# Kernel tuning notes

Measured on AMD Instinct MI355X. Metric: run time of the kernel, lower is better.

## Reference

```python
import jax, jax.numpy as jnp
import numpy as np

NUM_TILES = 32
N_HEAD = 4
D_MODEL = 256


def build_key_indices(n):
    # Mirrors the torch __init__ loop: row+column neighbors of token i on an n x n grid.
    key_indices = []
    for i in range(n * n):
        idx = []
        start = i // n
        end = i % n
        for j in range(n):
            idx.append(start * n + j)
            idx.append(end + n * j)
        idx.remove(i)  # i appears twice; one occurrence remains, matching torch
        key_indices.append(sorted(idx))
    return np.asarray(key_indices, dtype=np.int32)  # [T, 2n-1]


def setup_inputs() -> dict:
    key = jax.random.key(0)
    ks = jax.random.split(key, 5)
    B, T, D = 4, NUM_TILES ** 2, D_MODEL
    K = 2 * NUM_TILES - 1
    x = jax.random.normal(ks[0], (B, T, D), jnp.float32)
    scale = 1.0 / np.sqrt(D)
    Wq = jax.random.normal(ks[1], (D, D), jnp.float32) * scale  # [out, in] torch layout
    Wk = jax.random.normal(ks[2], (D, D), jnp.float32) * scale
    Wv = jax.random.normal(ks[3], (D, D), jnp.float32) * scale
    lim = np.sqrt(6.0 / (T + K))  # xavier_uniform
    wbias = jax.random.uniform(ks[4], (T, K), jnp.float32, -lim, lim)
    key_indices = jnp.asarray(build_key_indices(NUM_TILES))
    return {"x": x, "Wq": Wq, "Wk": Wk, "Wv": Wv, "wbias": wbias,
            "key_indices": key_indices}


def reference(x, Wq, Wk, Wv, wbias, key_indices):
    B, T, D = x.shape
    H = N_HEAD
    d = D // H
    # projections (torch Linear: x @ W.T), split heads -> [B,H,T,d]
    q = (x @ Wq.T).reshape(B, T, H, d).transpose(0, 2, 1, 3)
    k = (x @ Wk.T).reshape(B, T, H, d).transpose(0, 2, 1, 3)
    v = (x @ Wv.T).reshape(B, T, H, d).transpose(0, 2, 1, 3)

    ew = jnp.exp(wbias)          # [T, K]
    ek = jnp.exp(k)              # [B,H,T,d]
    kv = ek * v                  # [B,H,T,d]

    kv_g = kv[:, :, key_indices, :]   # gather -> [B,H,T,K,d]
    ek_g = ek[:, :, key_indices, :]   # gather -> [B,H,T,K,d]

    num = jnp.einsum('tk,bhtkd->bhtd', ew, kv_g)
    den = jnp.einsum('tk,bhtkd->bhtd', ew, ek_g)
    weighted = num / den

    out = jax.nn.sigmoid(q) * weighted          # [B,H,T,d]
    return out.transpose(0, 2, 1, 3).reshape(B, T, D)
```

## Files before the change

kernel.cpp:

```cpp
#include <hip/hip_runtime.h>
#include <math.h>

#define TT   1024
#define DD   256
#define KN   63
#define BB   4
#define MM   (BB * TT)

__global__ __launch_bounds__(256) void proj_kernel(
    const float* __restrict__ x,
    const float* __restrict__ Wq,
    const float* __restrict__ Wk,
    const float* __restrict__ Wv,
    float* __restrict__ P,
    float* __restrict__ EK,
    float* __restrict__ V)
{
    const int z = blockIdx.z;
    const float* __restrict__ W = (z == 0) ? Wq : (z == 1) ? Wk : Wv;
    float* __restrict__ outbuf  = (z == 0) ? P  : (z == 1) ? EK : V;

    __shared__ float xs[64][65];
    __shared__ float ws[64][65];

    const int tid = threadIdx.x;
    const int tx  = tid & 15;
    const int ty  = tid >> 4;
    const int m0  = blockIdx.x * 64;
    const int n0  = blockIdx.y * 64;

    float acc[4][4] = {};

    for (int kk = 0; kk < DD; kk += 64) {
        #pragma unroll
        for (int i = 0; i < 4; ++i) {
            const int l  = tid + 256 * i;
            const int r  = l >> 4;
            const int c4 = l & 15;
            float4 a = *reinterpret_cast<const float4*>(
                &x[(size_t)(m0 + r) * DD + kk + c4 * 4]);
            xs[r][c4 * 4 + 0] = a.x; xs[r][c4 * 4 + 1] = a.y;
            xs[r][c4 * 4 + 2] = a.z; xs[r][c4 * 4 + 3] = a.w;
            float4 b = *reinterpret_cast<const float4*>(
                &W[(size_t)(n0 + r) * DD + kk + c4 * 4]);
            ws[r][c4 * 4 + 0] = b.x; ws[r][c4 * 4 + 1] = b.y;
            ws[r][c4 * 4 + 2] = b.z; ws[r][c4 * 4 + 3] = b.w;
        }
        __syncthreads();

        #pragma unroll
        for (int k = 0; k < 64; ++k) {
            float a[4], b[4];
            #pragma unroll
            for (int i = 0; i < 4; ++i) a[i] = xs[ty * 4 + i][k];
            #pragma unroll
            for (int j = 0; j < 4; ++j) b[j] = ws[tx * 4 + j][k];
            #pragma unroll
            for (int i = 0; i < 4; ++i)
                #pragma unroll
                for (int j = 0; j < 4; ++j)
                    acc[i][j] += a[i] * b[j];
        }
        __syncthreads();
    }

    #pragma unroll
    for (int i = 0; i < 4; ++i) {
        const int r = m0 + ty * 4 + i;
        #pragma unroll
        for (int j = 0; j < 4; ++j) {
            const int c = n0 + tx * 4 + j;
            float v = acc[i][j];
            if (z == 0)      v = 1.0f / (1.0f + __expf(-v));
            else if (z == 1) v = __expf(v);
            outbuf[(size_t)r * DD + c] = v;
        }
    }
}

__global__ __launch_bounds__(256) void gather_kernel(
    const float* __restrict__ P,
    const float* __restrict__ EK,
    const float* __restrict__ V,
    const float* __restrict__ wbias,
    const int*   __restrict__ kidx,
    float* __restrict__ out)
{
    const int bt  = blockIdx.x;
    const int b   = bt >> 10;
    const int t   = bt & (TT - 1);
    const int tid = threadIdx.x;

    __shared__ float ews[KN];
    __shared__ int   idxs[KN];
    if (tid < KN) {
        ews[tid]  = __expf(wbias[t * KN + tid]);
        idxs[tid] = kidx[t * KN + tid];
    }
    __syncthreads();

    const size_t bbase = (size_t)b * TT * DD;
    float num = 0.0f, den = 0.0f;

    #pragma unroll 7
    for (int k = 0; k < KN; ++k) {
        const float  w    = ews[k];
        const size_t base = bbase + (size_t)idxs[k] * DD + tid;
        const float  e    = EK[base];
        const float  v    = V[base];
        den += w * e;
        num += w * e * v;
    }

    const size_t o = bbase + (size_t)t * DD + tid;
    out[o] = P[o] * num / den;
}

extern "C" void kernel_launch(void* const* d_in, const int* in_sizes, int n_in,
                              void* d_out, int out_size, void* d_ws, size_t ws_size,
                              hipStream_t stream) {
    const float* x     = (const float*)d_in[0];
    const float* Wq    = (const float*)d_in[1];
    const float* Wk    = (const float*)d_in[2];
    const float* Wv    = (const float*)d_in[3];
    const float* wbias = (const float*)d_in[4];
    const int*   kidx  = (const int*)d_in[5];
    float* out = (float*)d_out;

    float* P  = (float*)d_ws;
    float* EK = P  + (size_t)MM * DD;
    float* V  = EK + (size_t)MM * DD;

    dim3 g1(MM / 64, DD / 64, 3);
    proj_kernel<<<g1, dim3(256), 0, stream>>>(x, Wq, Wk, Wv, P, EK, V);

    gather_kernel<<<dim3(MM), dim3(256), 0, stream>>>(P, EK, V, wbias, kidx, out);
}
```

Baseline: 127.1 us.

## Use split-bf16 MFMA projections and separable row/column neighbor aggregation

Replaces the FP32 SIMT projection GEMM with bf16 MFMA, splitting inputs into high and low parts and using three products to keep near-FP32 accuracy. The per-token gather over 63 neighbours becomes a row pass and a column pass that stage a grid row or column in LDS and reuse it across 32 tokens. A prep kernel scatters exp(wbias) into dense row and column weight matrices. This adds two kernel launches and extra conversion traffic, and relies on the key indices having the row-plus-column grid structure, which the prep kernel decodes from kidx.

```diff
diff --git a/kernel.cpp b/kernel.cpp
--- a/kernel.cpp
+++ b/kernel.cpp
@@ -1,4 +1,5 @@
 #include <hip/hip_runtime.h>
+#include <hip/hip_bf16.h>
 #include <math.h>
 
 #define TT   1024
@@ -6,114 +7,268 @@
 #define KN   63
 #define BB   4
 #define MM   (BB * TT)
-
-__global__ __launch_bounds__(256) void proj_kernel(
-    const float* __restrict__ x,
-    const float* __restrict__ Wq,
-    const float* __restrict__ Wk,
-    const float* __restrict__ Wv,
-    float* __restrict__ P,
-    float* __restrict__ EK,
-    float* __restrict__ V)
-{
-    const int z = blockIdx.z;
-    const float* __restrict__ W = (z == 0) ? Wq : (z == 1) ? Wk : Wv;
-    float* __restrict__ outbuf  = (z == 0) ? P  : (z == 1) ? EK : V;
-
-    __shared__ float xs[64][65];
-    __shared__ float ws[64][65];
-
+#define NW   768
+
+typedef short bf16x8 __attribute__((ext_vector_type(8)));
+typedef float f32x4  __attribute__((ext_vector_type(4)));
+
+__device__ __forceinline__ unsigned short bf16bits(float f) {
+    __hip_bfloat16 h = __float2bfloat16(f);
+    return *reinterpret_cast<unsigned short*>(&h);
+}
+__device__ __forceinline__ float bf16tof(unsigned short u) {
+    __hip_bfloat16 h;
+    *reinterpret_cast<unsigned short*>(&h) = u;
+    return __bfloat162float(h);
+}
+
+__global__ __launch_bounds__(256) void prep_kernel(
+    const float* __restrict__ x,  const float* __restrict__ Wq,
+    const float* __restrict__ Wk, const float* __restrict__ Wv,
+    const float* __restrict__ wbias, const int* __restrict__ kidx,
+    __hip_bfloat16* __restrict__ xh, __hip_bfloat16* __restrict__ xl,
+    __hip_bfloat16* __restrict__ Wh, __hip_bfloat16* __restrict__ Wl,
+    float* __restrict__ Aw, float* __restrict__ Bw)
+{
+    const int bid = blockIdx.x, tid = threadIdx.x;
+    if (bid < 1024) {
+        const int e = bid * 1024 + tid * 4;
+        float4 v = *reinterpret_cast<const float4*>(&x[e]);
+        float vf[4] = {v.x, v.y, v.z, v.w};
+        ushort4 hh, ll;
+        unsigned short* hp = &hh.x;
+        unsigned short* lp = &ll.x;
+        #pragma unroll
+        for (int i = 0; i < 4; ++i) {
+            unsigned short h = bf16bits(vf[i]);
+            hp[i] = h;
+            lp[i] = bf16bits(vf[i] - bf16tof(h));
+        }
+        *reinterpret_cast<ushort4*>(xh + e) = hh;
+        *reinterpret_cast<ushort4*>(xl + e) = ll;
+    } else if (bid < 1216) {
+        const int e = (bid - 1024) * 1024 + tid * 4;
+        const int zz = e >> 16;
+        const float* __restrict__ Ws = (zz == 0) ? Wq : (zz == 1) ? Wk : Wv;
+        const int off = e & 65535;
+        float4 v = *reinterpret_cast<const float4*>(&Ws[off]);
+        float vf[4] = {v.x, v.y, v.z, v.w};
+        ushort4 hh, ll;
+        unsigned short* hp = &hh.x;
+        unsigned short* lp = &ll.x;
+        #pragma unroll
+        for (int i = 0; i < 4; ++i) {
+            unsigned short h = bf16bits(vf[i]);
+            hp[i] = h;
+            lp[i] = bf16bits(vf[i] - bf16tof(h));
+        }
+        *reinterpret_cast<ushort4*>(Wh + e) = hh;
+        *reinterpret_cast<ushort4*>(Wl + e) = ll;
+    } else {
+        __shared__ float wbuf[4][64];
+        const int wv = tid >> 6, lane = tid & 63;
+        const int t = (bid - 1216) * 4 + wv;
+        wbuf[wv][lane] = 0.0f;
+        __syncthreads();
+        if (lane < KN) {
+            const float w  = __expf(wbias[t * KN + lane]);
+            const int  idx = kidx[t * KN + lane];
+            const int  ir = idx >> 5, ic = idx & 31;
+            const int  rr = t >> 5;
+            if (ir == rr) wbuf[wv][ic] = w;
+            else          wbuf[wv][32 + ir] = w;
+        }
+        __syncthreads();
+        if (lane < 32) Aw[t * 32 + lane] = wbuf[wv][lane];
+        else           Bw[t * 32 + (lane - 32)] = wbuf[wv][lane - 32 + 32];
+    }
+}
+
+__device__ __forceinline__ void stage_tile(const __hip_bfloat16* __restrict__ src,
+                                           char* __restrict__ lds, int tid)
+{
+    #pragma unroll
+    for (int i = 0; i < 2; ++i) {
+        const int slot = tid + i * 256;
+        const int row = slot >> 2;
+        const int ks  = slot & 3;
+        int4 v = *reinterpret_cast<const int4*>(src + (size_t)row * DD + ks * 8);
+        *reinterpret_cast<int4*>(lds + row * 64 + ((ks ^ ((row >> 1) & 3)) << 4)) = v;
+    }
+}
+
+__global__ __launch_bounds__(256) void proj_mfma(
+    const __hip_bfloat16* __restrict__ xh, const __hip_bfloat16* __restrict__ xl,
+    const __hip_bfloat16* __restrict__ Wh, const __hip_bfloat16* __restrict__ Wl,
+    float* __restrict__ P, float* __restrict__ E, float* __restrict__ V)
+{
+    __shared__ char lds[32768];
     const int tid = threadIdx.x;
-    const int tx  = tid & 15;
-    const int ty  = tid >> 4;
-    const int m0  = blockIdx.x * 64;
-    const int n0  = blockIdx.y * 64;
-
-    float acc[4][4] = {};
-
-    for (int kk = 0; kk < DD; kk += 64) {
-        #pragma unroll
-        for (int i = 0; i < 4; ++i) {
-            const int l  = tid + 256 * i;
-            const int r  = l >> 4;
-            const int c4 = l & 15;
-            float4 a = *reinterpret_cast<const float4*>(
-                &x[(size_t)(m0 + r) * DD + kk + c4 * 4]);
-            xs[r][c4 * 4 + 0] = a.x; xs[r][c4 * 4 + 1] = a.y;
-            xs[r][c4 * 4 + 2] = a.z; xs[r][c4 * 4 + 3] = a.w;
-            float4 b = *reinterpret_cast<const float4*>(
-                &W[(size_t)(n0 + r) * DD + kk + c4 * 4]);
-            ws[r][c4 * 4 + 0] = b.x; ws[r][c4 * 4 + 1] = b.y;
-            ws[r][c4 * 4 + 2] = b.z; ws[r][c4 * 4 + 3] = b.w;
-        }
+    const int lane = tid & 63, wave = tid >> 6;
+    const int wr = wave >> 1, wc = wave & 1;
+    const int m0 = blockIdx.x * 128;
+    const int ny = blockIdx.y;
+    const int n0 = ny * 128;
+
+    f32x4 acc[4][4];
+    #pragma unroll
+    for (int i = 0; i < 4; ++i)
+        #pragma unroll
+        for (int j = 0; j < 4; ++j) acc[i][j] = (f32x4)0.0f;
+
+    const int kg = lane >> 4, li = lane & 15;
+
+    for (int kt = 0; kt < 8; ++kt) {
+        const int k0 = kt * 32;
+        stage_tile(xh + (size_t)m0 * DD + k0, lds,         tid);
+        stage_tile(xl + (size_t)m0 * DD + k0, lds + 8192,  tid);
+        stage_tile(Wh + (size_t)n0 * DD + k0, lds + 16384, tid);
+        stage_tile(Wl + (size_t)n0 * DD + k0, lds + 24576, tid);
         __syncthreads();
 
-        #pragma unroll
-        for (int k = 0; k < 64; ++k) {
-            float a[4], b[4];
+        bf16x8 bh[4], bl[4];
+        #pragma unroll
+        for (int fn = 0; fn < 4; ++fn) {
+            const int r   = wc * 64 + fn * 16 + li;
+            const int off = r * 64 + ((kg ^ ((r >> 1) & 3)) << 4);
+            bh[fn] = *reinterpret_cast<const bf16x8*>(lds + 16384 + off);
+            bl[fn] = *reinterpret_cast<const bf16x8*>(lds + 24576 + off);
+        }
+        #pragma unroll
+        for (int fm = 0; fm < 4; ++fm) {
+            const int r   = wr * 64 + fm * 16 + li;
+            const int off = r * 64 + ((kg ^ ((r >> 1) & 3)) << 4);
+            bf16x8 ah = *reinterpret_cast<const bf16x8*>(lds + off);
+            bf16x8 al = *reinterpret_cast<const bf16x8*>(lds + 8192 + off);
             #pragma unroll
-            for (int i = 0; i < 4; ++i) a[i] = xs[ty * 4 + i][k];
+            for (int fn = 0; fn < 4; ++fn) {
+                acc[fm][fn] = __builtin_amdgcn_mfma_f32_16x16x32_bf16(ah, bh[fn], acc[fm][fn], 0, 0, 0);
+                acc[fm][fn] = __builtin_amdgcn_mfma_f32_16x16x32_bf16(ah, bl[fn], acc[fm][fn], 0, 0, 0);
+                acc[fm][fn] = __builtin_amdgcn_mfma_f32_16x16x32_bf16(al, bh[fn], acc[fm][fn], 0, 0, 0);
+            }
+        }
+        __syncthreads();
+    }
+
+    const int region = ny >> 1;
+    float* __restrict__ ob = (region == 0) ? P : (region == 1) ? E : V;
+    const int ncol0 = (ny & 1) * 128;
+    const int lj = (lane >> 4) << 2;
+    #pragma unroll
+    for (int fm = 0; fm < 4; ++fm) {
+        #pragma unroll
+        for (int fn = 0; fn < 4; ++fn) {
+            const int mb = m0 + wr * 64 + fm * 16 + lj;
+            const int cc = ncol0 + wc * 64 + fn * 16 + li;
             #pragma unroll
-            for (int j = 0; j < 4; ++j) b[j] = ws[tx * 4 + j][k];
-            #pragma unroll
-            for (int i = 0; i < 4; ++i)
-                #pragma unroll
-                for (int j = 0; j < 4; ++j)
-                    acc[i][j] += a[i] * b[j];
-        }
-        __syncthreads();
-    }
+            for (int j = 0; j < 4; ++j) {
+                float v0 = acc[fm][fn][j];
+                if (region == 0)      v0 = 1.0f / (1.0f + __expf(-v0));
+                else if (region == 1) v0 = __expf(v0);
+                ob[(size_t)(mb + j) * DD + cc] = v0;
+            }
+        }
+    }
+}
+
+__global__ __launch_bounds__(256) void rowpass(
+    const float* __restrict__ E, const float* __restrict__ V,
+    const float* __restrict__ Aw, float* __restrict__ Nout, float* __restrict__ Dout)
+{
+    __shared__ float Et[32][132], Vt[32][132], At[32][36];
+    const int bid = blockIdx.x, tid = threadIdx.x;
+    const int dh = bid & 1, r = (bid >> 1) & 31, b = bid >> 6;
+    const size_t base = ((size_t)(b * TT + r * 32)) * DD + dh * 128;
 
     #pragma unroll
     for (int i = 0; i < 4; ++i) {
-        const int r = m0 + ty * 4 + i;
-        #pragma unroll
-        for (int j = 0; j < 4; ++j) {
-            const int c = n0 + tx * 4 + j;
-            float v = acc[i][j];
-            if (z == 0)      v = 1.0f / (1.0f + __expf(-v));
-            else if (z == 1) v = __expf(v);
-            outbuf[(size_t)r * DD + c] = v;
-        }
-    }
-}
-
-__global__ __launch_bounds__(256) void gather_kernel(
-    const float* __restrict__ P,
-    const float* __restrict__ EK,
-    const float* __restrict__ V,
-    const float* __restrict__ wbias,
-    const int*   __restrict__ kidx,
-    float* __restrict__ out)
-{
-    const int bt  = blockIdx.x;
-    const int b   = bt >> 10;
-    const int t   = bt & (TT - 1);
-    const int tid = threadIdx.x;
-
-    __shared__ float ews[KN];
-    __shared__ int   idxs[KN];
-    if (tid < KN) {
-        ews[tid]  = __expf(wbias[t * KN + tid]);
-        idxs[tid] = kidx[t * KN + tid];
+        const int slot = tid + i * 256;
+        const int row = slot >> 5, c4 = (slot & 31) * 4;
+        *reinterpret_cast<f32x4*>(&Et[row][c4]) =
+            *reinterpret_cast<const f32x4*>(&E[base + (size_t)row * DD + c4]);
+        *reinterpret_cast<f32x4*>(&Vt[row][c4]) =
+            *reinterpret_cast<const f32x4*>(&V[base + (size_t)row * DD + c4]);
+    }
+    {
+        const int c = tid >> 3, j4 = (tid & 7) * 4;
+        *reinterpret_cast<f32x4*>(&At[c][j4]) =
+            *reinterpret_cast<const f32x4*>(&Aw[(size_t)(r * 32 + c) * 32 + j4]);
     }
     __syncthreads();
 
-    const size_t bbase = (size_t)b * TT * DD;
-    float num = 0.0f, den = 0.0f;
-
-    #pragma unroll 7
-    for (int k = 0; k < KN; ++k) {
-        const float  w    = ews[k];
-        const size_t base = bbase + (size_t)idxs[k] * DD + tid;
-        const float  e    = EK[base];
-        const float  v    = V[base];
-        den += w * e;
-        num += w * e * v;
-    }
-
-    const size_t o = bbase + (size_t)t * DD + tid;
-    out[o] = P[o] * num / den;
+    const int dq = tid & 31, cg = tid >> 5;
+    f32x4 num[4], den[4];
+    #pragma unroll
+    for (int ci = 0; ci < 4; ++ci) { num[ci] = (f32x4)0.0f; den[ci] = (f32x4)0.0f; }
+
+    for (int j = 0; j < 32; ++j) {
+        f32x4 e = *reinterpret_cast<const f32x4*>(&Et[j][dq * 4]);
+        f32x4 v = *reinterpret_cast<const f32x4*>(&Vt[j][dq * 4]);
+        f32x4 ev = e * v;
+        #pragma unroll
+        for (int ci = 0; ci < 4; ++ci) {
+            const float w = At[cg * 4 + ci][j];
+            den[ci] += e * w;
+            num[ci] += ev * w;
+        }
+    }
+    #pragma unroll
+    for (int ci = 0; ci < 4; ++ci) {
+        const size_t o = ((size_t)(b * TT + r * 32 + cg * 4 + ci)) * DD + dh * 128 + dq * 4;
+        *reinterpret_cast<f32x4*>(&Nout[o]) = num[ci];
+        *reinterpret_cast<f32x4*>(&Dout[o]) = den[ci];
+    }
+}
+
+__global__ __launch_bounds__(256) void colpass(
+    const float* __restrict__ E, const float* __restrict__ V,
+    const float* __restrict__ Bw, const float* __restrict__ P,
+    const float* __restrict__ Drow, float* __restrict__ out)
+{
+    __shared__ float Et[32][132], Vt[32][132], Bt[32][36];
+    const int bid = blockIdx.x, tid = threadIdx.x;
+    const int dh = bid & 1, c = (bid >> 1) & 31, b = bid >> 6;
+
+    #pragma unroll
+    for (int i = 0; i < 4; ++i) {
+        const int slot = tid + i * 256;
+        const int j = slot >> 5, c4 = (slot & 31) * 4;
+        const size_t g = ((size_t)(b * TT + j * 32 + c)) * DD + dh * 128 + c4;
+        *reinterpret_cast<f32x4*>(&Et[j][c4]) = *reinterpret_cast<const f32x4*>(&E[g]);
+        *reinterpret_cast<f32x4*>(&Vt[j][c4]) = *reinterpret_cast<const f32x4*>(&V[g]);
+    }
+    {
+        const int rr = tid >> 3, j4 = (tid & 7) * 4;
+        *reinterpret_cast<f32x4*>(&Bt[rr][j4]) =
+            *reinterpret_cast<const f32x4*>(&Bw[(size_t)(rr * 32 + c) * 32 + j4]);
+    }
+    __syncthreads();
+
+    const int dq = tid & 31, rg = tid >> 5;
+    f32x4 num[4], den[4];
+    #pragma unroll
+    for (int ri = 0; ri < 4; ++ri) { num[ri] = (f32x4)0.0f; den[ri] = (f32x4)0.0f; }
+
+    for (int j = 0; j < 32; ++j) {
+        f32x4 e = *reinterpret_cast<const f32x4*>(&Et[j][dq * 4]);
+        f32x4 v = *reinterpret_cast<const f32x4*>(&Vt[j][dq * 4]);
+        f32x4 ev = e * v;
+        #pragma unroll
+        for (int ri = 0; ri < 4; ++ri) {
+            const float w = Bt[rg * 4 + ri][j];
+            den[ri] += e * w;
+            num[ri] += ev * w;
+        }
+    }
+    #pragma unroll
+    for (int ri = 0; ri < 4; ++ri) {
+        const size_t o = ((size_t)(b * TT + (rg * 4 + ri) * 32 + c)) * DD + dh * 128 + dq * 4;
+        f32x4 nr = *reinterpret_cast<const f32x4*>(&out[o]);
+        f32x4 dr = *reinterpret_cast<const f32x4*>(&Drow[o]);
+        f32x4 p  = *reinterpret_cast<const f32x4*>(&P[o]);
+        f32x4 res = p * (num[ri] + nr) / (den[ri] + dr);
+        *reinterpret_cast<f32x4*>(&out[o]) = res;
+    }
 }
 
 extern "C" void kernel_launch(void* const* d_in, const int* in_sizes, int n_in,
@@ -125,14 +280,21 @@
     const float* Wv    = (const float*)d_in[3];
     const float* wbias = (const float*)d_in[4];
     const int*   kidx  = (const int*)d_in[5];
-    float* out = (float*)d_out;
 
     float* P  = (float*)d_ws;
-    float* EK = P  + (size_t)MM * DD;
-    float* V  = EK + (size_t)MM * DD;
-
-    dim3 g1(MM / 64, DD / 64, 3);
-    proj_kernel<<<g1, dim3(256), 0, stream>>>(x, Wq, Wk, Wv, P, EK, V);
-
-    gather_kernel<<<dim3(MM), dim3(256), 0, stream>>>(P, EK, V, wbias, kidx, out);
-}
+    float* E  = P + 1048576;
+    float* V  = E + 1048576;
+    float* Aw = V + 1048576;
+    float* Bw = Aw + 32768;
+    __hip_bfloat16* xh = (__hip_bfloat16*)(Bw + 32768);
+    __hip_bfloat16* xl = xh + 1048576;
+    __hip_bfloat16* Wh = xl + 1048576;
+    __hip_bfloat16* Wl = Wh + 196608;
+    float* Dbuf = (float*)xh;
+
+    prep_kernel<<<1472, 256, 0, stream>>>(x, Wq, Wk, Wv, wbias, kidx,
+                                          xh, xl, Wh, Wl, Aw, Bw);
+    proj_mfma<<<dim3(32, 6), 256, 0, stream>>>(xh, xl, Wh, Wl, P, E, V);
+    rowpass<<<256, 256, 0, stream>>>(E, V, Aw, (float*)d_out, Dbuf);
+    colpass<<<256, 256, 0, stream>>>(E, V, Bw, P, Dbuf, (float*)d_out);
+}
```

Result: faster. 102.7 us (-19.1%).
